# Kernel tuning notes

Hardware: AMD Instinct MI355X
Metric: run time of the kernel (lower is better)

Reference implementation:

```python
import jax, jax.numpy as jnp
import numpy as np

N = 262144
FC = 256
XYZ_FREQ, DIR_FREQ = 10, 4
IN_XYZ = 3 + 3 * 2 * XYZ_FREQ  # 63
IN_DIR = 3 + 3 * 2 * DIR_FREQ  # 27
SKIP = 4


def posenc(p, n_freqs):
    bands = 2.0 ** jnp.arange(n_freqs, dtype=p.dtype)          # [F]
    xb = p[..., None, :] * bands[:, None]                       # [N, F, 3]
    sc = jnp.stack([jnp.sin(xb), jnp.cos(xb)], axis=-2)         # [N, F, 2, 3]
    return jnp.concatenate([p, sc.reshape(p.shape[0], n_freqs * 6)], axis=-1)


def setup_inputs() -> dict:
    key = jax.random.key(0)
    ks = jax.random.split(key, 32)
    s = 0.05
    inp = {"x": jax.random.normal(ks[0], (N, 6), jnp.float32)}
    dims_in = [IN_XYZ] + [FC + IN_XYZ if i == SKIP else FC for i in range(1, 8)]
    for i in range(8):
        inp[f"w{i}"] = jax.random.normal(ks[1 + i], (dims_in[i], FC), jnp.float32) * s
        inp[f"b{i}"] = jnp.zeros((FC,), jnp.float32)
    inp["w_final"] = jax.random.normal(ks[10], (FC, FC), jnp.float32) * s
    inp["b_final"] = jnp.zeros((FC,), jnp.float32)
    inp["w_sigma"] = jax.random.normal(ks[11], (FC, 1), jnp.float32) * s
    inp["b_sigma"] = jnp.zeros((1,), jnp.float32)
    inp["w_rgb1"] = jax.random.normal(ks[12], (FC + IN_DIR, FC // 2), jnp.float32) * s
    inp["b_rgb1"] = jnp.zeros((FC // 2,), jnp.float32)
    inp["w_rgb2"] = jax.random.normal(ks[13], (FC // 2, 3), jnp.float32) * s
    inp["b_rgb2"] = jnp.zeros((3,), jnp.float32)
    return inp


def reference(x, w0, b0, w1, b1, w2, b2, w3, b3, w4, b4, w5, b5, w6, b6, w7, b7,
              w_final, b_final, w_sigma, b_sigma, w_rgb1, b_rgb1, w_rgb2, b_rgb2):
    input_xyz = posenc(x[:, :3], XYZ_FREQ)   # [N, 63]
    input_dir = posenc(x[:, 3:], DIR_FREQ)   # [N, 27]
    ws = [w0, w1, w2, w3, w4, w5, w6, w7]
    bs = [b0, b1, b2, b3, b4, b5, b6, b7]
    h = input_xyz
    for i in range(8):
        if i == SKIP:
            h = jnp.concatenate([input_xyz, h], axis=-1)
        h = jax.nn.relu(h @ ws[i] + bs[i])
    sigma = h @ w_sigma + b_sigma                               # [N, 1]
    final = h @ w_final + b_final                               # [N, 256]
    dir_enc = jnp.concatenate([final, input_dir], axis=-1)      # [N, 283]
    hidden = jax.nn.relu(dir_enc @ w_rgb1 + b_rgb1)
    rgb = jax.nn.sigmoid(hidden @ w_rgb2 + b_rgb2)              # [N, 3]
    return jnp.concatenate([rgb, sigma], axis=-1)               # [N, 4]
```

## Files before the change

kernel.cpp:

```cpp
#include <hip/hip_runtime.h>
#include <hip/hip_fp16.h>
#include <stdint.h>

typedef unsigned int   uint32;
typedef unsigned short ushort_t;
typedef _Float16 half8   __attribute__((ext_vector_type(8)));
typedef float    floatx4 __attribute__((ext_vector_type(4)));

#define DEVINL __device__ __forceinline__

#define HS 256
#define XSTR 72
#define N_FRAGS 1172

__device__ __align__(16) ushort_t g_ws[(size_t)N_FRAGS * 512];

DEVINL ushort_t f2h_u(float v) { return __half_as_ushort(__float2half(v)); }

DEVINL uint4 make_frag_qword(const float* __restrict__ W, int Kr, int Nr,
                             int skip63, int kt, int nt, int q, int cc)
{
    const int n = nt*16 + cc;
    uint32 pk[4];
    #pragma unroll
    for (int jj = 0; jj < 4; ++jj) {
        ushort_t h2[2];
        #pragma unroll
        for (int e = 0; e < 2; ++e) {
            const int k = kt*32 + q*8 + jj*2 + e;
            float v = 0.f;
            if (n < Nr) {
                if (skip63) {
                    if (k != 63) { const int rr = (k < 63) ? k : (k - 1); v = W[(size_t)rr*Nr + n]; }
                } else if (k < Kr) {
                    v = W[(size_t)k*Nr + n];
                }
            }
            h2[e] = f2h_u(v);
        }
        pk[jj] = (uint32)h2[0] | ((uint32)h2[1] << 16);
    }
    return make_uint4(pk[0], pk[1], pk[2], pk[3]);
}

__global__ __launch_bounds__(256) void prep_weights(
    const float* __restrict__ w0, const float* __restrict__ w1,
    const float* __restrict__ w2, const float* __restrict__ w3,
    const float* __restrict__ w4, const float* __restrict__ w5,
    const float* __restrict__ w6, const float* __restrict__ w7,
    const float* __restrict__ wf, const float* __restrict__ wsig,
    const float* __restrict__ wr1, const float* __restrict__ wr2)
{
    int gid  = blockIdx.x * 256 + threadIdx.x;
    int frag = gid >> 6;
    if (frag >= N_FRAGS) return;
    int lane = gid & 63;
    const int foff[13] = {0,32,160,288,416,576,704,832,960,1088,1096,1168,1172};
    const int NT[12]   = {16,16,16,16,16,16,16,16,16,1,8,1};
    const int KR[12]   = {63,256,256,256,319,256,256,256,256,256,283,128};
    const int NR[12]   = {256,256,256,256,256,256,256,256,256,1,128,3};
    const float* WP[12] = {w0,w1,w2,w3,w4,w5,w6,w7,wf,wsig,wr1,wr2};
    int t = 0;
    while (frag >= foff[t+1]) ++t;
    int fl = frag - foff[t];
    int nt = fl % NT[t];
    int kt = fl / NT[t];
    uint4 pk = make_frag_qword(WP[t], KR[t], NR[t], (t == 4) ? 1 : 0, kt, nt,
                               lane >> 4, lane & 15);
    *(uint4*)(g_ws + (size_t)frag*512 + lane*8) = pk;
}

template <int NT_W, int KT, int KT_SPLIT, int NTT, int S0, int S1,
          bool SWZ0, bool SWZ1>
DEVINL void run_layer(const ushort_t* __restrict__ wsrc,
                      const ushort_t* __restrict__ in0,
                      const ushort_t* __restrict__ in1,
                      int lane, int q, int cc, int nt_lo,
                      const floatx4 (&binit)[NT_W], floatx4 (&acc)[4][NT_W])
{
    half8 bfr[2][4];
    half8 afr[2][NT_W];
    const int sx = cc & 7;

    auto loadk = [&](int kt, int buf) {
        if (kt < KT_SPLIT) {
            if (SWZ0) {
                const ushort_t* p = in0 + cc*HS + (((kt*4 + q) ^ sx) * 8);
                #pragma unroll
                for (int rt = 0; rt < 4; ++rt)
                    bfr[buf][rt] = *(const half8*)(p + rt*16*HS);
            } else {
                const ushort_t* p = in0 + cc*S0 + q*8;
                #pragma unroll
                for (int rt = 0; rt < 4; ++rt)
                    bfr[buf][rt] = *(const half8*)(p + kt*32 + rt*16*S0);
            }
        } else {
            const int kk = kt - KT_SPLIT;
            if (SWZ1) {
                const ushort_t* p = in1 + cc*HS + (((kk*4 + q) ^ sx) * 8);
                #pragma unroll
                for (int rt = 0; rt < 4; ++rt)
                    bfr[buf][rt] = *(const half8*)(p + rt*16*HS);
            } else {
                const ushort_t* p = in1 + cc*S1 + q*8;
                #pragma unroll
                for (int rt = 0; rt < 4; ++rt)
                    bfr[buf][rt] = *(const half8*)(p + kk*32 + rt*16*S1);
            }
        }
        const ushort_t* wb = wsrc + (size_t)(kt*NTT + nt_lo)*512 + lane*8;
        #pragma unroll
        for (int nt = 0; nt < NT_W; ++nt)
            afr[buf][nt] = *(const half8*)(wb + nt*512);
    };

    loadk(0, 0);
    #pragma unroll
    for (int kt = 0; kt < KT; ++kt) {
        const int cur = kt & 1;
        if (kt + 1 < KT) loadk(kt + 1, cur ^ 1);
        #pragma unroll
        for (int nt = 0; nt < NT_W; ++nt)
            #pragma unroll
            for (int rt = 0; rt < 4; ++rt)
                acc[rt][nt] = __builtin_amdgcn_mfma_f32_16x16x32_f16(
                    afr[cur][nt], bfr[cur][rt],
                    (kt == 0) ? binit[nt] : acc[rt][nt], 0, 0, 0);
    }
}

template <int NT_W, bool RELU>
DEVINL void epilogue_h(floatx4 (&acc)[4][NT_W], int nt_lo,
                       ushort_t* __restrict__ shh, int q, int cc)
{
    const int sx = cc & 7;
    #pragma unroll
    for (int nt = 0; nt < NT_W; ++nt) {
        const int ch = (((nt_lo + nt)*2 + (q >> 1)) ^ sx);
        ushort_t* p = shh + cc*HS + ch*8 + (q & 1)*4;
        #pragma unroll
        for (int rt = 0; rt < 4; ++rt) {
            floatx4 v = acc[rt][nt];
            if (RELU) {
                v.x = fmaxf(v.x, 0.f); v.y = fmaxf(v.y, 0.f);
                v.z = fmaxf(v.z, 0.f); v.w = fmaxf(v.w, 0.f);
            }
            uint2 u;
            u.x = __builtin_bit_cast(uint32, __builtin_amdgcn_cvt_pkrtz(v.x, v.y));
            u.y = __builtin_bit_cast(uint32, __builtin_amdgcn_cvt_pkrtz(v.z, v.w));
            *(uint2*)(p + rt*16*HS) = u;
        }
    }
}

__global__ __launch_bounds__(256, 3) void nerf_fused(
    const float* __restrict__ x,
    const float* __restrict__ b0, const float* __restrict__ b1,
    const float* __restrict__ b2, const float* __restrict__ b3,
    const float* __restrict__ b4, const float* __restrict__ b5,
    const float* __restrict__ b6, const float* __restrict__ b7,
    const float* __restrict__ bf, const float* __restrict__ bsig,
    const float* __restrict__ br1, const float* __restrict__ br2,
    float* __restrict__ out)
{
    __shared__ __align__(16) ushort_t shh[64*HS];
    __shared__ __align__(16) ushort_t shx[64*XSTR];

    const int tid  = threadIdx.x;
    const int wave = tid >> 6, lane = tid & 63;
    const int q = lane >> 4, cc = lane & 15;
    const int r0 = blockIdx.x * 64;
    const ushort_t* ws = g_ws;

    float xd0, xd1, xd2;

    {
        const int r = lane;
        const float* xr = x + (size_t)(r0 + r)*6;
        xd0 = xr[3]; xd1 = xr[4]; xd2 = xr[5];
        for (int j = wave; j < 30; j += 4) {
            int f = j/3, a = j%3;
            float v = xr[a] * (float)(1 << f);
            shx[r*XSTR + 3 + f*6 + a]     = f2h_u(sinf(v));
            shx[r*XSTR + 3 + f*6 + 3 + a] = f2h_u(cosf(v));
        }
        if (wave == 0) {
            #pragma unroll
            for (int a = 0; a < 3; ++a)
                shx[r*XSTR + a] = f2h_u(xr[a]);
            shx[r*XSTR + 63] = 0;
        }
    }
    __syncthreads();

    const float* BS[8] = {b0,b1,b2,b3,b4,b5,b6,b7};
    const int WO[8] = {0,16384,81920,147456,212992,294912,360448,425984};
    const int nt_lo4 = wave * 4;
    const floatx4 vz = {0.f, 0.f, 0.f, 0.f};

    floatx4 acc[4][4];
    floatx4 bl[4];

    #pragma unroll
    for (int nt = 0; nt < 4; ++nt)
        bl[nt] = *(const floatx4*)(b0 + (nt_lo4 + nt)*16 + q*4);
    run_layer<4,2,2,16,XSTR,XSTR,false,false>(ws + WO[0], shx, shx, lane, q, cc, nt_lo4, bl, acc);
    epilogue_h<4,true>(acc, nt_lo4, shh, q, cc);
    __syncthreads();

    #pragma unroll
    for (int l = 1; l < 8; ++l) {
        if (l == 5) {
            const int r = lane;
            const float xdv[3] = {xd0, xd1, xd2};
            for (int j = wave; j < 12; j += 4) {
                int f = j/3, a = j%3;
                float v = xdv[a] * (float)(1 << f);
                shx[r*XSTR + 3 + f*6 + a]     = f2h_u(sinf(v));
                shx[r*XSTR + 3 + f*6 + 3 + a] = f2h_u(cosf(v));
            }
            if (wave == 0) {
                #pragma unroll
                for (int a = 0; a < 3; ++a)
                    shx[r*XSTR + a] = f2h_u(xdv[a]);
                #pragma unroll
                for (int kq = 27; kq < 32; ++kq) shx[r*XSTR + kq] = 0;
            }
        }
        #pragma unroll
        for (int nt = 0; nt < 4; ++nt)
            bl[nt] = *(const floatx4*)(BS[l] + (nt_lo4 + nt)*16 + q*4);
        if (l == 4)
            run_layer<4,10,2,16,XSTR,HS,false,true>(ws + WO[4], shx, shh, lane, q, cc, nt_lo4, bl, acc);
        else
            run_layer<4,8,8,16,HS,HS,true,true>(ws + WO[l], shh, shh, lane, q, cc, nt_lo4, bl, acc);
        __syncthreads();
        epilogue_h<4,true>(acc, nt_lo4, shh, q, cc);
        __syncthreads();
    }

    if (wave == 0) {
        floatx4 sacc[4][1];
        const floatx4 bz[1] = {vz};
        run_layer<1,8,8,1,HS,HS,true,true>(ws + 557056, shh, shh, lane, q, cc, 0, bz, sacc);
        if (q == 0) {
            const float bs_ = bsig[0];
            #pragma unroll
            for (int rt = 0; rt < 4; ++rt)
                out[(size_t)(r0 + rt*16 + cc)*4 + 3] = sacc[rt][0].x + bs_;
        }
    }

    #pragma unroll
    for (int nt = 0; nt < 4; ++nt)
        bl[nt] = *(const floatx4*)(bf + (nt_lo4 + nt)*16 + q*4);
    run_layer<4,8,8,16,HS,HS,true,true>(ws + 491520, shh, shh, lane, q, cc, nt_lo4, bl, acc);
    __syncthreads();
    epilogue_h<4,false>(acc, nt_lo4, shh, q, cc);
    __syncthreads();

    {
        floatx4 racc[4][2];
        floatx4 bl2[2];
        #pragma unroll
        for (int nt = 0; nt < 2; ++nt)
            bl2[nt] = *(const floatx4*)(br1 + (wave*2 + nt)*16 + q*4);
        run_layer<2,9,8,8,HS,XSTR,true,false>(ws + 561152, shh, shx, lane, q, cc, wave*2, bl2, racc);
        __syncthreads();
        epilogue_h<2,true>(racc, wave*2, shh, q, cc);
        __syncthreads();
    }

    if (wave == 0) {
        floatx4 cacc[4][1];
        const floatx4 bz[1] = {vz};
        run_layer<1,4,4,1,HS,HS,true,true>(ws + 598016, shh, shh, lane, q, cc, 0, bz, cacc);
        if (q == 0) {
            const float c0 = br2[0], c1 = br2[1], c2 = br2[2];
            #pragma unroll
            for (int rt = 0; rt < 4; ++rt) {
                const size_t o = (size_t)(r0 + rt*16 + cc)*4;
                out[o+0] = 1.f/(1.f + expf(-(cacc[rt][0].x + c0)));
                out[o+1] = 1.f/(1.f + expf(-(cacc[rt][0].y + c1)));
                out[o+2] = 1.f/(1.f + expf(-(cacc[rt][0].z + c2)));
            }
        }
    }
}

extern "C" void kernel_launch(void* const* d_in, const int* in_sizes, int n_in,
                              void* d_out, int out_size, void* d_ws, size_t ws_size,
                              hipStream_t stream)
{
    const float* x  = (const float*)d_in[0];
    const float* w0 = (const float*)d_in[1];  const float* b0 = (const float*)d_in[2];
    const float* w1 = (const float*)d_in[3];  const float* b1 = (const float*)d_in[4];
    const float* w2 = (const float*)d_in[5];  const float* b2 = (const float*)d_in[6];
    const float* w3 = (const float*)d_in[7];  const float* b3 = (const float*)d_in[8];
    const float* w4 = (const float*)d_in[9];  const float* b4 = (const float*)d_in[10];
    const float* w5 = (const float*)d_in[11]; const float* b5 = (const float*)d_in[12];
    const float* w6 = (const float*)d_in[13]; const float* b6 = (const float*)d_in[14];
    const float* w7 = (const float*)d_in[15]; const float* b7 = (const float*)d_in[16];
    const float* wf = (const float*)d_in[17]; const float* bf = (const float*)d_in[18];
    const float* wsg= (const float*)d_in[19]; const float* bsg= (const float*)d_in[20];
    const float* wr1= (const float*)d_in[21]; const float* br1= (const float*)d_in[22];
    const float* wr2= (const float*)d_in[23]; const float* br2= (const float*)d_in[24];
    float* out = (float*)d_out;
    const int N = in_sizes[0] / 6;

    prep_weights<<<(N_FRAGS*64 + 255)/256, 256, 0, stream>>>(
        w0,w1,w2,w3,w4,w5,w6,w7,wf,wsg,wr1,wr2);
    nerf_fused<<<N/64, 256, 0, stream>>>(
        x, b0,b1,b2,b3,b4,b5,b6,b7, bf,bsg, br1,br2, out);
}
```

Baseline: 397.4 us.

## Split each 64-row tile across 8 waves with 2 column tiles per wave

The fused NeRF MLP kernel now launches 512 threads per block instead of 256, so each wave owns 2 output column tiles (32 columns) instead of 4, and the RGB hidden layer uses one tile per wave. Positional encoding loops stride by 8 waves. The aim is more waves per block to hide LDS/MFMA latency and to cut accumulator registers per thread. In exchange each wave reuses each A-fragment load for fewer MFMAs, which raises LDS read traffic per FLOP, and launch bounds drop to 2 blocks per CU.

```diff
diff --git a/kernel.cpp b/kernel.cpp
--- a/kernel.cpp
+++ b/kernel.cpp
@@ -154,7 +154,7 @@
     }
 }
 
-__global__ __launch_bounds__(256, 3) void nerf_fused(
+__global__ __launch_bounds__(512, 2) void nerf_fused(
     const float* __restrict__ x,
     const float* __restrict__ b0, const float* __restrict__ b1,
     const float* __restrict__ b2, const float* __restrict__ b3,
@@ -179,7 +179,7 @@
         const int r = lane;
         const float* xr = x + (size_t)(r0 + r)*6;
         xd0 = xr[3]; xd1 = xr[4]; xd2 = xr[5];
-        for (int j = wave; j < 30; j += 4) {
+        for (int j = wave; j < 30; j += 8) {
             int f = j/3, a = j%3;
             float v = xr[a] * (float)(1 << f);
             shx[r*XSTR + 3 + f*6 + a]     = f2h_u(sinf(v));
@@ -196,17 +196,17 @@
 
     const float* BS[8] = {b0,b1,b2,b3,b4,b5,b6,b7};
     const int WO[8] = {0,16384,81920,147456,212992,294912,360448,425984};
-    const int nt_lo4 = wave * 4;
+    const int nt_lo2 = wave * 2;
     const floatx4 vz = {0.f, 0.f, 0.f, 0.f};
 
-    floatx4 acc[4][4];
-    floatx4 bl[4];
-
-    #pragma unroll
-    for (int nt = 0; nt < 4; ++nt)
-        bl[nt] = *(const floatx4*)(b0 + (nt_lo4 + nt)*16 + q*4);
-    run_layer<4,2,2,16,XSTR,XSTR,false,false>(ws + WO[0], shx, shx, lane, q, cc, nt_lo4, bl, acc);
-    epilogue_h<4,true>(acc, nt_lo4, shh, q, cc);
+    floatx4 acc[4][2];
+    floatx4 bl[2];
+
+    #pragma unroll
+    for (int nt = 0; nt < 2; ++nt)
+        bl[nt] = *(const floatx4*)(b0 + (nt_lo2 + nt)*16 + q*4);
+    run_layer<2,2,2,16,XSTR,XSTR,false,false>(ws + WO[0], shx, shx, lane, q, cc, nt_lo2, bl, acc);
+    epilogue_h<2,true>(acc, nt_lo2, shh, q, cc);
     __syncthreads();
 
     #pragma unroll
@@ -214,7 +214,7 @@
         if (l == 5) {
             const int r = lane;
             const float xdv[3] = {xd0, xd1, xd2};
-            for (int j = wave; j < 12; j += 4) {
+            for (int j = wave; j < 12; j += 8) {
                 int f = j/3, a = j%3;
                 float v = xdv[a] * (float)(1 << f);
                 shx[r*XSTR + 3 + f*6 + a]     = f2h_u(sinf(v));
@@ -229,14 +229,14 @@
             }
         }
         #pragma unroll
-        for (int nt = 0; nt < 4; ++nt)
-            bl[nt] = *(const floatx4*)(BS[l] + (nt_lo4 + nt)*16 + q*4);
+        for (int nt = 0; nt < 2; ++nt)
+            bl[nt] = *(const floatx4*)(BS[l] + (nt_lo2 + nt)*16 + q*4);
         if (l == 4)
-            run_layer<4,10,2,16,XSTR,HS,false,true>(ws + WO[4], shx, shh, lane, q, cc, nt_lo4, bl, acc);
+            run_layer<2,10,2,16,XSTR,HS,false,true>(ws + WO[4], shx, shh, lane, q, cc, nt_lo2, bl, acc);
         else
-            run_layer<4,8,8,16,HS,HS,true,true>(ws + WO[l], shh, shh, lane, q, cc, nt_lo4, bl, acc);
+            run_layer<2,8,8,16,HS,HS,true,true>(ws + WO[l], shh, shh, lane, q, cc, nt_lo2, bl, acc);
         __syncthreads();
-        epilogue_h<4,true>(acc, nt_lo4, shh, q, cc);
+        epilogue_h<2,true>(acc, nt_lo2, shh, q, cc);
         __syncthreads();
     }
 
@@ -253,22 +253,20 @@
     }
 
     #pragma unroll
-    for (int nt = 0; nt < 4; ++nt)
-        bl[nt] = *(const floatx4*)(bf + (nt_lo4 + nt)*16 + q*4);
-    run_layer<4,8,8,16,HS,HS,true,true>(ws + 491520, shh, shh, lane, q, cc, nt_lo4, bl, acc);
+    for (int nt = 0; nt < 2; ++nt)
+        bl[nt] = *(const floatx4*)(bf + (nt_lo2 + nt)*16 + q*4);
+    run_layer<2,8,8,16,HS,HS,true,true>(ws + 491520, shh, shh, lane, q, cc, nt_lo2, bl, acc);
     __syncthreads();
-    epilogue_h<4,false>(acc, nt_lo4, shh, q, cc);
+    epilogue_h<2,false>(acc, nt_lo2, shh, q, cc);
     __syncthreads();
 
     {
-        floatx4 racc[4][2];
-        floatx4 bl2[2];
-        #pragma unroll
-        for (int nt = 0; nt < 2; ++nt)
-            bl2[nt] = *(const floatx4*)(br1 + (wave*2 + nt)*16 + q*4);
-        run_layer<2,9,8,8,HS,XSTR,true,false>(ws + 561152, shh, shx, lane, q, cc, wave*2, bl2, racc);
+        floatx4 racc[4][1];
+        floatx4 bl1[1];
+        bl1[0] = *(const floatx4*)(br1 + wave*16 + q*4);
+        run_layer<1,9,8,8,HS,XSTR,true,false>(ws + 561152, shh, shx, lane, q, cc, wave, bl1, racc);
         __syncthreads();
-        epilogue_h<2,true>(racc, wave*2, shh, q, cc);
+        epilogue_h<1,true>(racc, wave, shh, q, cc);
         __syncthreads();
     }
 
@@ -311,6 +309,6 @@
 
     prep_weights<<<(N_FRAGS*64 + 255)/256, 256, 0, stream>>>(
         w0,w1,w2,w3,w4,w5,w6,w7,wf,wsg,wr1,wr2);
-    nerf_fused<<<N/64, 256, 0, stream>>>(
+    nerf_fused<<<N/64, 512, 0, stream>>>(
         x, b0,b1,b2,b3,b4,b5,b6,b7, bf,bsg, br1,br2, out);
 }
```

Result: slower. 455.6 us (+14.7%).
